# Kernel optimization log

Measured on AMD Instinct MI355X. Metric: run time of the kernel, lower is better.

The kernel has to match this reference:

```python
import jax, jax.numpy as jnp
import numpy as np

jax.config.update("jax_enable_x64", True)

B, N, M_EQ, D_INEQ = 64, 128, 32, 64
RHO = 1.0
THRES = 1e-5
MAX_ITERS = 5000  # safety cap (original loops until relative objective change <= 1e-5)


def setup_inputs() -> dict:
    key = jax.random.key(0)
    kL, kq, kG, kA, kx0, ks = jax.random.split(key, 6)
    L = jax.random.normal(kL, (B, N, N))
    Q = jnp.einsum('bij,bkj->bik', L, L) / N + jnp.eye(N)  # SPD, well-conditioned
    q = jax.random.normal(kq, (B, N))
    G = jax.random.normal(kG, (B, D_INEQ, N))
    A = jax.random.normal(kA, (B, M_EQ, N))
    x0 = jax.random.normal(kx0, (B, N))
    slack = jax.random.uniform(ks, (B, D_INEQ)) + 0.1
    h = jnp.einsum('bdn,bn->bd', G, x0) + slack  # strictly feasible ineq
    b = jnp.einsum('bmn,bn->bm', A, x0)          # feasible eq
    f32 = jnp.float32
    return {"Q": Q.astype(f32), "q": q.astype(f32), "G": G.astype(f32),
            "h": h.astype(f32), "A": A.astype(f32), "b": b.astype(f32)}


def _alt_diff_batch(Q, q, G, h, A, b):
    """Batched Alt-Diff ADMM QP solve; returns (x [B,n], dx/dq [B,n,n])."""
    Bb, n = q.shape
    d = h.shape[1]
    m = b.shape[1]
    dt = Q.dtype
    AtA = jnp.einsum('bmi,bmj->bij', A, A)
    GtG = jnp.einsum('bdi,bdj->bij', G, G)
    R = -jnp.linalg.inv(Q + RHO * AtA + RHO * GtG)
    ATb = RHO * jnp.einsum('bmn,bm->bn', A, b)
    GTh = RHO * jnp.einsum('bdn,bd->bn', G, h)
    eye = jnp.eye(n, dtype=dt)

    def obj(x):
        return 0.5 * jnp.einsum('bi,bij,bj->b', x, Q, x) + jnp.einsum('bi,bi->b', q, x)

    init = dict(
        xk=jnp.zeros((Bb, n), dt), sk=jnp.zeros((Bb, d), dt),
        lamb=jnp.zeros((Bb, m), dt), nu=jnp.zeros((Bb, d), dt),
        dxk=jnp.zeros((Bb, n, n), dt), dsk=jnp.zeros((Bb, d, n), dt),
        dlamb=jnp.zeros((Bb, m, n), dt), dnu=jnp.zeros((Bb, d, n), dt),
        res_prev=jnp.full((Bb,), 1000.0, dt),   # res = [1000, -100] init
        res_cur=jnp.full((Bb,), -100.0, dt),
        done=jnp.zeros((Bb,), bool),
        it=jnp.zeros((), jnp.int32),
    )

    def cond(s):
        return jnp.logical_and(jnp.any(~s["done"]), s["it"] < MAX_ITERS)

    def body(s):
        xk = jnp.einsum('bij,bj->bi', R,
                        q + jnp.einsum('bmn,bm->bn', A, s["lamb"])
                          + jnp.einsum('bdn,bd->bn', G, s["nu"]) - ATb
                          + RHO * jnp.einsum('bdn,bd->bn', G, s["sk"]) - GTh)
        dxk = jnp.einsum('bij,bjk->bik', R,
                         eye + jnp.einsum('bmn,bmk->bnk', A, s["dlamb"])
                             + jnp.einsum('bdn,bdk->bnk', G, s["dnu"])
                             + RHO * jnp.einsum('bdn,bdk->bnk', G, s["dsk"]))
        Gx = jnp.einsum('bdn,bn->bd', G, xk)
        sk = jax.nn.relu(-(1.0 / RHO) * s["nu"] - (Gx - h))
        sgn = (sk > 0).astype(dt)  # sgn applied to already-relu'd sk, as in source
        dsk = (-1.0 / RHO) * sgn[:, :, None] * (s["dnu"] + RHO * jnp.einsum('bdn,bnk->bdk', G, dxk))
        lamb = s["lamb"] + RHO * (jnp.einsum('bmn,bn->bm', A, xk) - b)
        dlamb = s["dlamb"] + RHO * jnp.einsum('bmn,bnk->bmk', A, dxk)
        nu = s["nu"] + RHO * (Gx + sk - h)
        dnu = s["dnu"] + RHO * (jnp.einsum('bdn,bnk->bdk', G, dxk) + dsk)
        res_new = obj(xk)

        keep = s["done"]

        def sel(old, new):
            mask = keep.reshape((-1,) + (1,) * (new.ndim - 1))
            return jnp.where(mask, old, new)

        res_prev = jnp.where(keep, s["res_prev"], s["res_cur"])
        res_cur = jnp.where(keep, s["res_cur"], res_new)
        done = keep | (jnp.abs((res_cur - res_prev) / res_prev) <= THRES)
        return dict(
            xk=sel(s["xk"], xk), sk=sel(s["sk"], sk),
            lamb=sel(s["lamb"], lamb), nu=sel(s["nu"], nu),
            dxk=sel(s["dxk"], dxk), dsk=sel(s["dsk"], dsk),
            dlamb=sel(s["dlamb"], dlamb), dnu=sel(s["dnu"], dnu),
            res_prev=res_prev, res_cur=res_cur, done=done, it=s["it"] + 1,
        )

    final = jax.lax.while_loop(cond, body, init)
    return final["xk"], final["dxk"]


def reference(Q, q, G, h, A, b):
    out_dtype = q.dtype
    f64 = jnp.float64
    x, _dx = _alt_diff_batch(Q.astype(f64), q.astype(f64), G.astype(f64),
                             h.astype(f64), A.astype(f64), b.astype(f64))
    return x.astype(out_dtype)
```

## Files before the change

### kernel.cpp

```cpp
#include <hip/hip_runtime.h>

#define NN 128
#define ME 32
#define DI 64
#define NZ 96
#define ROWD 130
#define MAXIT 5000

#define OFF_UN 16640
#define ROWB  (OFF_UN)
#define COLB  (OFF_UN + 256)
#define PPK   (OFF_UN)
#define TVX   (OFF_UN + 512)
#define TV16  (OFF_UN + 640)
#define FLG   (OFF_UN + 672)
#define YBUF  (OFF_UN)
#define KBUF  (OFF_UN + 1536)
#define CPART (OFF_UN + 1024)
#define VP    (OFF_UN + 1280)
#define BASEV (OFF_UN + 1792)
#define QBV   (OFF_UN + 1888)
#define FPART (OFF_UN + 1024)
#define RHSV  (OFF_UN + 1280)
#define XPART (OFF_UN + 1408)
#define CB    (OFF_UN + 2688)
#define QBUF  (OFF_UN + 2816)
#define V1    (OFF_UN + 2944)
#define V2    (OFF_UN + 3072)
#define HB    (OFF_UN + 3200)
#define BB    (OFF_UN + 3264)
#define CST   (OFF_UN + 3296)
#define ZBF   (OFF_UN + 3304)
#define LDS_DBL (OFF_UN + 3400)

typedef __attribute__((ext_vector_type(2))) float f32x2;

__device__ __forceinline__ float rlf(float v, int lane) {
  return __uint_as_float((unsigned)__builtin_amdgcn_readlane((int)__float_as_uint(v), lane));
}
__device__ __forceinline__ f32x2 fma2(f32x2 a, f32x2 b, f32x2 c) {
  return __builtin_elementwise_fma(a, b, c);
}

#define MV2(PA, ZS, L0) {                                                  \
    f32x2 z0 = { rlf(ZS, L0), rlf(ZS, (L0)+1) };                           \
    A0 = fma2(Kp[PA], z0, A0); B0 = fma2(Kp2[PA], z0, B0);                 \
    f32x2 z1 = { rlf(ZS, (L0)+2), rlf(ZS, (L0)+3) };                       \
    A1 = fma2(Kp[(PA)+1], z1, A1); B1 = fma2(Kp2[(PA)+1], z1, B1); }

#define CPYRANGE(LBASE, KBASE, CNT)                                        \
  _Pragma("unroll") for (int j = 0; j < (CNT); ++j) {                      \
    const int lj = (LBASE) + j, kc = (KBASE) + j;                          \
    float va = (float)ldsd[KBUF + kc*NZ + l];                              \
    float vb = (float)ldsd[KBUF + kc*NZ + 64 + lm];                        \
    if ((lj & 1) == 0) { Kp[lj>>1].x = va; Kp2[lj>>1].x = vb; }            \
    else               { Kp[lj>>1].y = va; Kp2[lj>>1].y = vb; }            \
  }

__global__ __launch_bounds__(256, 1) void altdiff_kernel(
    const float* __restrict__ Qg, const float* __restrict__ qg,
    const float* __restrict__ Gg, const float* __restrict__ hg,
    const float* __restrict__ Ag, const float* __restrict__ bg,
    float* __restrict__ out)
{
  extern __shared__ double ldsd[];

  const int bidx = blockIdx.x;
  const int tid  = threadIdx.x;
  const int w    = tid >> 6;
  const int l    = tid & 63;
  const int lm   = l & 31;
  const int ia   = tid & 127;
  const int hh   = tid >> 7;

  const float* Qb = Qg + (size_t)bidx * NN * NN;
  const float* Ab = Ag + (size_t)bidx * ME * NN;
  const float* Gb = Gg + (size_t)bidx * DI * NN;
  const float* qb = qg + (size_t)bidx * NN;
  const float* hb = hg + (size_t)bidx * DI;
  const float* bv = bg + (size_t)bidx * ME;

  if (tid < DI) ldsd[HB + tid] = (double)hb[tid];
  else if (tid < DI + ME) ldsd[BB + tid - DI] = (double)bv[tid - DI];
  if (tid >= 128) ldsd[QBUF + tid - 128] = (double)qb[tid - 128];

  const int r = tid >> 4, c = tid & 15;
  double acc[8][8];

  {
    const float4* Q4 = (const float4*)Qb;
#pragma unroll
    for (int rr = 0; rr < 8; ++rr) {
      float4 q0 = Q4[((8*r+rr) << 5) + 2*c];
      float4 q1 = Q4[((8*r+rr) << 5) + 2*c + 1];
      acc[rr][0]=(double)q0.x; acc[rr][1]=(double)q0.y; acc[rr][2]=(double)q0.z; acc[rr][3]=(double)q0.w;
      acc[rr][4]=(double)q1.x; acc[rr][5]=(double)q1.y; acc[rr][6]=(double)q1.z; acc[rr][7]=(double)q1.w;
    }
    const float4* A4 = (const float4*)Ab;
    for (int m = 0; m < ME; ++m) {
      float4 u0 = A4[(m << 5) + 2*r], u1 = A4[(m << 5) + 2*r + 1];
      float4 v0 = A4[(m << 5) + 2*c], v1 = A4[(m << 5) + 2*c + 1];
      double uu[8] = {(double)u0.x,(double)u0.y,(double)u0.z,(double)u0.w,
                      (double)u1.x,(double)u1.y,(double)u1.z,(double)u1.w};
      double vv[8] = {(double)v0.x,(double)v0.y,(double)v0.z,(double)v0.w,
                      (double)v1.x,(double)v1.y,(double)v1.z,(double)v1.w};
#pragma unroll
      for (int rr = 0; rr < 8; ++rr)
#pragma unroll
        for (int cc = 0; cc < 8; ++cc)
          acc[rr][cc] = fma(uu[rr], vv[cc], acc[rr][cc]);
    }
    const float4* G4 = (const float4*)Gb;
    for (int d = 0; d < DI; ++d) {
      float4 u0 = G4[(d << 5) + 2*r], u1 = G4[(d << 5) + 2*r + 1];
      float4 v0 = G4[(d << 5) + 2*c], v1 = G4[(d << 5) + 2*c + 1];
      double uu[8] = {(double)u0.x,(double)u0.y,(double)u0.z,(double)u0.w,
                      (double)u1.x,(double)u1.y,(double)u1.z,(double)u1.w};
      double vv[8] = {(double)v0.x,(double)v0.y,(double)v0.z,(double)v0.w,
                      (double)v1.x,(double)v1.y,(double)v1.z,(double)v1.w};
#pragma unroll
      for (int rr = 0; rr < 8; ++rr)
#pragma unroll
        for (int cc = 0; cc < 8; ++cc)
          acc[rr][cc] = fma(uu[rr], vv[cc], acc[rr][cc]);
    }
  }

  {
    if (r == 0) {
#pragma unroll
      for (int cc = 0; cc < 8; ++cc) ldsd[ROWB + 8*c + cc] = acc[0][cc];
    }
    if (c == 0) {
#pragma unroll
      for (int rr = 0; rr < 8; ++rr) ldsd[COLB + 8*r + rr] = acc[rr][0];
    }
    __syncthreads();
    for (int k = 0; k < NN; ++k) {
      const int pb = (k & 1) << 7;
      const int krt = k >> 3, kcl = k & 7;
      double rowk[8], colv[8];
#pragma unroll
      for (int cc = 0; cc < 8; ++cc) rowk[cc] = ldsd[ROWB + pb + 8*c + cc];
#pragma unroll
      for (int rr = 0; rr < 8; ++rr) colv[rr] = ldsd[COLB + pb + 8*r + rr];
      const double dkk  = ldsd[ROWB + pb + k];
      const double rcpd = 1.0 / dkk;
      double rdv[8];
#pragma unroll
      for (int cc = 0; cc < 8; ++cc) rdv[cc] = rowk[cc] * rcpd;
      const bool pivR = (r == krt), pivC = (c == krt);
#pragma unroll
      for (int rr = 0; rr < 8; ++rr) {
        const double cv = colv[rr] * rcpd;
        const bool pr = pivR && (rr == kcl);
#pragma unroll
        for (int cc = 0; cc < 8; ++cc) {
          double gen = fma(-cv, rowk[cc], acc[rr][cc]);
          acc[rr][cc] = pr ? rdv[cc] : gen;
        }
      }
      if (pivC) {
#pragma unroll
        for (int cc = 0; cc < 8; ++cc) if (cc == kcl) {
#pragma unroll
          for (int rr = 0; rr < 8; ++rr) {
            const bool pr2 = pivR && (rr == kcl);
            acc[rr][cc] = pr2 ? -rcpd : colv[rr] * rcpd;
          }
        }
      }
      if (k < NN - 1) {
        const int pb2 = ((k + 1) & 1) << 7;
        const int krt2 = (k + 1) >> 3, kcl2 = (k + 1) & 7;
        if (r == krt2) {
#pragma unroll
          for (int rr = 0; rr < 8; ++rr) if (rr == kcl2) {
#pragma unroll
            for (int cc = 0; cc < 8; ++cc) ldsd[ROWB + pb2 + 8*c + cc] = acc[rr][cc];
          }
        }
        if (c == krt2) {
#pragma unroll
          for (int cc = 0; cc < 8; ++cc) if (cc == kcl2) {
#pragma unroll
            for (int rr = 0; rr < 8; ++rr) ldsd[COLB + pb2 + 8*r + rr] = acc[rr][cc];
          }
        }
      }
      __syncthreads();
    }
#pragma unroll
    for (int rr = 0; rr < 8; ++rr) {
      double2* dst = (double2*)(ldsd + (8*r+rr)*ROWD + 8*c);
#pragma unroll
      for (int t = 0; t < 4; ++t) dst[t] = make_double2(acc[rr][2*t], acc[rr][2*t+1]);
    }
  }
  __syncthreads();

  f32x2 Kp[14], Kp2[14];
  for (int blk = 0; blk < 8; ++blk) {
    {
      const float* gp[6];
#pragma unroll
      for (int jj = 0; jj < 6; ++jj) {
        int it = 12*blk + 6*hh + jj;
        gp[jj] = (it < DI) ? (Gb + it*NN) : (Ab + (it - DI)*NN);
      }
      double a2[6] = {0,0,0,0,0,0};
#pragma unroll 4
      for (int t = 0; t < NN; ++t) {
        double rv = ldsd[t*ROWD + ia];
#pragma unroll
        for (int jj = 0; jj < 6; ++jj)
          a2[jj] = fma(rv, (double)gp[jj][t], a2[jj]);
      }
      double2* yst = (double2*)(ldsd + YBUF + ia*12 + 6*hh);
#pragma unroll
      for (int p = 0; p < 3; ++p) yst[p] = make_double2(a2[2*p], a2[2*p+1]);
    }
    __syncthreads();
    {
      const int r2 = (ia < NZ) ? ia : 0;
      const float* brow = (r2 < DI) ? (Gb + r2*NN) : (Ab + (r2 - DI)*NN);
      double a2[6] = {0,0,0,0,0,0};
#pragma unroll 4
      for (int t = 0; t < NN; ++t) {
        double bvv = (double)brow[t];
        const double2* yr = (const double2*)(ldsd + YBUF + t*12 + 6*hh);
        double2 y0 = yr[0], y1 = yr[1], y2 = yr[2];
        a2[0] = fma(bvv, y0.x, a2[0]); a2[1] = fma(bvv, y0.y, a2[1]);
        a2[2] = fma(bvv, y1.x, a2[2]); a2[3] = fma(bvv, y1.y, a2[3]);
        a2[4] = fma(bvv, y2.x, a2[4]); a2[5] = fma(bvv, y2.y, a2[5]);
      }
      if (ia < NZ) {
#pragma unroll
        for (int jj = 0; jj < 6; ++jj) ldsd[KBUF + (6*hh + jj)*NZ + ia] = a2[jj];
      }
    }
    __syncthreads();
    if (w == 0) {
      if (blk == 0)      { CPYRANGE(0,  0, 12) }
      else if (blk == 1) { CPYRANGE(12, 0, 12) }
      else if (blk == 2) { CPYRANGE(24, 0, 4) }
    } else if (w == 1) {
      if (blk == 2)      { CPYRANGE(0,  4, 8) }
      else if (blk == 3) { CPYRANGE(8,  0, 12) }
      else if (blk == 4) { CPYRANGE(20, 0, 8) }
    } else if (w == 2) {
      if (blk == 4)      { CPYRANGE(0,  8, 4) }
      else if (blk == 5) { CPYRANGE(4,  0, 12) }
      else if (blk == 6) { CPYRANGE(16, 0, 8) }
    } else {
      if (blk == 6)      { CPYRANGE(0,  8, 4) }
      else if (blk == 7) { CPYRANGE(4,  0, 12) }
    }
    __syncthreads();
  }

  {
    double s = 0;
#pragma unroll 8
    for (int jc = 0; jc < 48; ++jc) {
      int j = 48*hh + jc;
      double coef = (j < DI) ? ldsd[HB + j] : ldsd[BB + j - DI];
      const float* src = (j < DI) ? (Gb + j*NN) : (Ab + (j - DI)*NN);
      s = fma(-(double)src[ia], coef, s);
    }
    ldsd[CPART + hh*128 + ia] = s;
  }
  __syncthreads();
  if (tid < NN) ldsd[CB + tid] = ldsd[QBUF + tid] + ldsd[CPART + tid] + ldsd[CPART + 128 + tid];
  __syncthreads();

  {
    double a = 0, b2 = 0;
#pragma unroll 4
    for (int tt = 0; tt < 64; ++tt) {
      int t = 64*hh + tt;
      double rv = ldsd[t*ROWD + ia];
      a  = fma(rv, ldsd[CB + t], a);
      b2 = fma(rv, ldsd[QBUF + t], b2);
    }
    ldsd[VP + hh*128 + ia] = a;
    ldsd[VP + 256 + hh*128 + ia] = b2;
  }
  __syncthreads();
  if (tid < NN) {
    ldsd[V1 + tid] = ldsd[VP + tid] + ldsd[VP + 128 + tid];
    ldsd[V2 + tid] = ldsd[VP + 256 + tid] + ldsd[VP + 384 + tid];
  }
  __syncthreads();

  {
    const int r2 = (ia < NZ) ? ia : 0;
    const float* brow = (r2 < DI) ? (Gb + r2*NN) : (Ab + (r2 - DI)*NN);
    const int voff = hh ? V2 : V1;
    double s = 0;
#pragma unroll 4
    for (int t = 0; t < NN; ++t) s = fma((double)brow[t], ldsd[voff + t], s);
    if (ia < NZ) ldsd[(hh ? QBV : BASEV) + ia] = s;
  }
  if (w == 0) {
    double pc = ldsd[V1+l]*ldsd[CB+l]   + ldsd[V1+64+l]*ldsd[CB+64+l];
    double pq = ldsd[V1+l]*ldsd[QBUF+l] + ldsd[V1+64+l]*ldsd[QBUF+64+l];
#pragma unroll
    for (int off = 32; off >= 1; off >>= 1) { pc += __shfl_xor(pc, off); pq += __shfl_xor(pq, off); }
    if (l == 0) { ldsd[CST] = pc; ldsd[CST+1] = pq; }
  }
  __syncthreads();

  const double baseA = ldsd[BASEV + l];
  const double baseB = ldsd[BASEV + 64 + lm];
  const double qvA   = ldsd[QBV + l];
  const double qvB   = ldsd[QBV + 64 + lm];
  const double hb2   = ldsd[HB + l] - baseA;
  const double bb2   = baseB - ldsd[BB + lm];
  const double S_uc  = ldsd[CST], S_qu = ldsd[CST + 1];
  double hnb = hb2, lb = bb2;
  float hnbf = (float)hnb, lbf = (float)lb;
  float zplo = 0.f, zphi = 0.f;
  float zAlo = 0.f, zAhi = 0.f, zBlo = 0.f, zBhi = 0.f, zClo = 0.f, zChi = 0.f;
  double res_prev = 1000.0, res_cur = -100.0;

  {
    *(float2*)&ldsd[PPK + w*64 + l] = make_float2(0.f, 0.f);
    if (tid == 0) { ldsd[FLG] = 0.0; ldsd[FLG + 1] = 0.0; }
  }

  for (int it = 0; it < MAXIT + 3; ++it) {
    __syncthreads();
    const int buf = it & 1, nbuf = buf ^ 1;
    const int bprev = nbuf;
    const double fl = ldsd[FLG + bprev];
    const float2* pb = (const float2*)(ldsd + PPK + buf*256);
    float2 p0 = pb[l], p1 = pb[64 + l], p2 = pb[128 + l], p3 = pb[192 + l];
    double a0 = 0, a1 = 0, a2 = 0, a3 = 0;
    double t1v[16];
    if (w == 3) {
      const int g = l & 15;
      const double* tq = ldsd + TVX + bprev*64;
      a0 = tq[g]; a1 = tq[g + 16]; a2 = tq[g + 32]; a3 = tq[g + 48];
      const double2* tp = (const double2*)(ldsd + TV16 + bprev*16);
#pragma unroll
      for (int u = 0; u < 8; ++u) { double2 vv = tp[u]; t1v[2*u] = vv.x; t1v[2*u+1] = vv.y; }
    }
    float slo = (p0.x + p1.x) + (p2.x + p3.x);
    float tf   = hnbf - slo;
    float zflo = fabsf(tf);
    float shi = 0.f, zfhi = 0.f;
    if (w >= 2) {
      shi  = (p0.y + p1.y) + (p2.y + p3.y);
      zfhi = lbf + shi;
    }
    if (it >= 3 && fl != 0.0) break;
    if (w == 3) { zClo = zBlo; zChi = zBhi; zBlo = zAlo; zBhi = zAhi; zAlo = zplo; zAhi = zphi; }
    if (it < MAXIT) {
      double t = hnb - (double)slo;
      hnb = hb2 + fmin(t, 0.0);
      hnbf = (float)hnb;
      if (w >= 2) {
        double lamn = lb + (double)shi;
        lb = lamn + bb2;
        lbf = (float)lb;
      }
      if (w == 3) { zplo = zflo; zphi = zfhi; }
      f32x2 A0 = {0.f, 0.f}, A1 = A0, B0 = A0, B1 = A0;
      if (w == 0) {
        MV2(0,  zflo, 0)  MV2(2,  zflo, 4)  MV2(4,  zflo, 8)  MV2(6,  zflo, 12)
        MV2(8,  zflo, 16) MV2(10, zflo, 20) MV2(12, zflo, 24)
      } else if (w == 1) {
        MV2(0,  zflo, 28) MV2(2,  zflo, 32) MV2(4,  zflo, 36) MV2(6,  zflo, 40)
        MV2(8,  zflo, 44) MV2(10, zflo, 48) MV2(12, zflo, 52)
      } else if (w == 2) {
        MV2(0,  zflo, 56) MV2(2,  zflo, 60)
        MV2(4,  zfhi, 0)  MV2(6,  zfhi, 4)  MV2(8,  zfhi, 8)  MV2(10, zfhi, 12)
      } else {
        MV2(0,  zfhi, 16) MV2(2,  zfhi, 20) MV2(4,  zfhi, 24) MV2(6,  zfhi, 28)
      }
      f32x2 As = A0 + A1, Bs = B0 + B1;
      *(float2*)&ldsd[PPK + nbuf*256 + w*64 + l] = make_float2(As.x + As.y, Bs.x + Bs.y);
      if (w == 3) {
        double yf  = (double)slo + baseA;
        double zAl = (double)zAlo;
        double tvl = fma(qvA, zAl, -0.5*(zAl*(baseA + yf) + yf*yf));
        double yfB = (double)shi + baseB;
        double zAh = (double)zAhi;
        double tvh = fma(qvB, zAh, -0.5*(zAh*(baseB + yfB) + yfB*yfB));
        ldsd[TVX + buf*64 + l] = tvl + ((l < 32) ? tvh : 0.0);
      }
    }
    if (w == 3) {
      if (l < 16 && it >= 1 && it <= MAXIT)
        ldsd[TV16 + buf*16 + l] = (a0 + a1) + (a2 + a3);
      if (it >= 2 && it <= MAXIT + 1) {
        double s1 = ((t1v[0] + t1v[1]) + (t1v[2] + t1v[3])) + ((t1v[4] + t1v[5]) + (t1v[6] + t1v[7]));
        double s2 = ((t1v[8] + t1v[9]) + (t1v[10] + t1v[11])) + ((t1v[12] + t1v[13]) + (t1v[14] + t1v[15]));
        double obj = (s1 + s2) - 0.5*S_uc + S_qu;
        res_prev = res_cur; res_cur = obj;
        if (l == 0)
          ldsd[FLG + buf] = (fabs(res_cur - res_prev) <= 1e-5 * fabs(res_prev)) ? 1.0 : 0.0;
      }
    }
  }

  if (w == 3) {
    ldsd[ZBF + l] = (double)zClo;
    if (l < 32) ldsd[ZBF + 64 + l] = (double)zChi;
  }
  __syncthreads();
  {
    double s = 0;
#pragma unroll 8
    for (int jc = 0; jc < 48; ++jc) {
      int j = 48*hh + jc;
      double zj = ldsd[ZBF + j];
      const float* src = (j < DI) ? (Gb + j*NN) : (Ab + (j - DI)*NN);
      s = fma((double)src[ia], zj, s);
    }
    ldsd[FPART + hh*128 + ia] = s;
  }
  __syncthreads();
  if (tid < NN) ldsd[RHSV + tid] = ldsd[CB + tid] + ldsd[FPART + tid] + ldsd[FPART + 128 + tid];
  __syncthreads();
  {
    double s = 0;
#pragma unroll 4
    for (int tt = 0; tt < 64; ++tt) {
      int t = 64*hh + tt;
      s = fma(ldsd[t*ROWD + ia], ldsd[RHSV + t], s);
    }
    ldsd[XPART + hh*128 + ia] = s;
  }
  __syncthreads();
  if (tid < NN)
    out[(size_t)bidx * NN + tid] = (float)(ldsd[XPART + tid] + ldsd[XPART + 128 + tid]);
}

extern "C" void kernel_launch(void* const* d_in, const int* in_sizes, int n_in,
                              void* d_out, int out_size, void* d_ws, size_t ws_size,
                              hipStream_t stream) {
  (void)in_sizes; (void)n_in; (void)out_size; (void)d_ws; (void)ws_size;
  const float* Q = (const float*)d_in[0];
  const float* q = (const float*)d_in[1];
  const float* G = (const float*)d_in[2];
  const float* h = (const float*)d_in[3];
  const float* A = (const float*)d_in[4];
  const float* b = (const float*)d_in[5];
  float* out = (float*)d_out;
  const size_t lds_bytes = (size_t)LDS_DBL * sizeof(double);
  altdiff_kernel<<<dim3(64), dim3(256), lds_bytes, stream>>>(Q, q, G, h, A, b, out);
}
```

Measured before the change: 685.9 us.

## Process two QP problems per workgroup with interleaved ADMM iterations

Each workgroup now handles two batch elements. It builds both problems' operators into separate register sets, then runs their ADMM iterations interleaved in one loop, so the serial per-iteration latency chain of one problem can hide the other's. The final solve uses a precomputed R*B^T stored in the workspace instead of recomputing it. This halves the grid to 32 blocks, doubles the register pressure and the setup work done per block, and adds global workspace traffic.

Result: slower. 1.297 ms (+89.0%).

```diff
diff --git a/kernel.cpp b/kernel.cpp
--- a/kernel.cpp
+++ b/kernel.cpp
@@ -7,31 +7,34 @@
 #define ROWD 130
 #define MAXIT 5000
 
+#define PPK_A   0
+#define PPK_B   384
+#define ZEXLF_A 1536
+#define ZEXHF_A 1664
+#define ZEXLF_B 1728
+#define ZEXHF_B 1856
+#define TVX_A   960
+#define TVX_B   1088
+#define TV16_A  1216
+#define TV16_B  1248
+#define FLG_A   1280
+#define FLG_B   1282
+#define ZBF_A   1284
+#define ZBF_B   1380
 #define OFF_UN 16640
 #define ROWB  (OFF_UN)
 #define COLB  (OFF_UN + 256)
-#define PPK   (OFF_UN)
-#define TVX   (OFF_UN + 512)
-#define TV16  (OFF_UN + 640)
-#define FLG   (OFF_UN + 672)
 #define YBUF  (OFF_UN)
-#define KBUF  (OFF_UN + 1536)
-#define CPART (OFF_UN + 1024)
-#define VP    (OFF_UN + 1280)
-#define BASEV (OFF_UN + 1792)
-#define QBV   (OFF_UN + 1888)
-#define FPART (OFF_UN + 1024)
-#define RHSV  (OFF_UN + 1280)
-#define XPART (OFF_UN + 1408)
-#define CB    (OFF_UN + 2688)
-#define QBUF  (OFF_UN + 2816)
-#define V1    (OFF_UN + 2944)
-#define V2    (OFF_UN + 3072)
-#define HB    (OFF_UN + 3200)
-#define BB    (OFF_UN + 3264)
-#define CST   (OFF_UN + 3296)
-#define ZBF   (OFF_UN + 3304)
-#define LDS_DBL (OFF_UN + 3400)
+#define KBUFF (2*(OFF_UN + 1536))
+#define CPART (OFF_UN)
+#define CBT   (OFF_UN + 256)
+#define QBUF  (OFF_UN + 384)
+#define VP    (OFF_UN + 512)
+#define V2T   (OFF_UN + 1024)
+#define FPART (OFF_UN)
+#define PBASE (OFF_UN + 2112)
+#define PCH   418
+#define LDS_DBL (PBASE + 2*PCH)
 
 typedef __attribute__((ext_vector_type(2))) float f32x2;
 
@@ -42,28 +45,55 @@
   return __builtin_elementwise_fma(a, b, c);
 }
 
-#define MV2(PA, ZS, L0) {                                                  \
-    f32x2 z0 = { rlf(ZS, L0), rlf(ZS, (L0)+1) };                           \
-    A0 = fma2(Kp[PA], z0, A0); B0 = fma2(Kp2[PA], z0, B0);                 \
-    f32x2 z1 = { rlf(ZS, (L0)+2), rlf(ZS, (L0)+3) };                       \
-    A1 = fma2(Kp[(PA)+1], z1, A1); B1 = fma2(Kp2[(PA)+1], z1, B1); }
-
-#define CPYRANGE(LBASE, KBASE, CNT)                                        \
-  _Pragma("unroll") for (int j = 0; j < (CNT); ++j) {                      \
-    const int lj = (LBASE) + j, kc = (KBASE) + j;                          \
-    float va = (float)ldsd[KBUF + kc*NZ + l];                              \
-    float vb = (float)ldsd[KBUF + kc*NZ + 64 + lm];                        \
-    if ((lj & 1) == 0) { Kp[lj>>1].x = va; Kp2[lj>>1].x = vb; }            \
-    else               { Kp[lj>>1].y = va; Kp2[lj>>1].y = vb; }            \
+#define MV2(KP, KP2, PA, ZS, L0) {                                          \
+    f32x2 z0 = { rlf(ZS, L0), rlf(ZS, (L0)+1) };                            \
+    A0 = fma2(KP[PA], z0, A0); B0 = fma2(KP2[PA], z0, B0);                  \
+    f32x2 z1 = { rlf(ZS, (L0)+2), rlf(ZS, (L0)+3) };                        \
+    A1 = fma2(KP[(PA)+1], z1, A1); B1 = fma2(KP2[(PA)+1], z1, B1); }
+
+#define BURST_LO_A(KP, KP2, Z)                              \
+    MV2(KP,KP2,0,Z,0)  MV2(KP,KP2,2,Z,4)  MV2(KP,KP2,4,Z,8)  MV2(KP,KP2,6,Z,12) \
+    MV2(KP,KP2,8,Z,16) MV2(KP,KP2,10,Z,20) MV2(KP,KP2,12,Z,24) MV2(KP,KP2,14,Z,28)
+#define BURST_LO_B(KP, KP2, Z)                             \
+    MV2(KP,KP2,0,Z,32) MV2(KP,KP2,2,Z,36) MV2(KP,KP2,4,Z,40) MV2(KP,KP2,6,Z,44) \
+    MV2(KP,KP2,8,Z,48) MV2(KP,KP2,10,Z,52) MV2(KP,KP2,12,Z,56) MV2(KP,KP2,14,Z,60)
+#define BURST_HI(KP, KP2, Z)                             \
+    MV2(KP,KP2,0,Z,0)  MV2(KP,KP2,2,Z,4)  MV2(KP,KP2,4,Z,8)  MV2(KP,KP2,6,Z,12) \
+    MV2(KP,KP2,8,Z,16) MV2(KP,KP2,10,Z,20) MV2(KP,KP2,12,Z,24) MV2(KP,KP2,14,Z,28)
+
+#define CPYRANGE(KP, KP2, LBASE, KBASE, CNT)                                \
+  _Pragma("unroll") for (int j = 0; j < (CNT); ++j) {                       \
+    const int lj = (LBASE) + j, kc = (KBASE) + j;                           \
+    float va = ldsf[KBUFF + kc*NZ + l];                                     \
+    float vb = ldsf[KBUFF + kc*NZ + 64 + lm];                               \
+    if ((lj & 1) == 0) { KP[lj>>1].x = va; KP2[lj>>1].x = vb; }             \
+    else               { KP[lj>>1].y = va; KP2[lj>>1].y = vb; }             \
+  }
+
+#define KCOPY_ARMS(KP, KP2)                                                 \
+  if (w == 0) {                                                             \
+    if (blk == 0)      { CPYRANGE(KP,KP2,0,  0, 12) }                       \
+    else if (blk == 1) { CPYRANGE(KP,KP2,12, 0, 12) }                       \
+    else if (blk == 2) { CPYRANGE(KP,KP2,24, 0, 8) }                        \
+  } else if (w == 1) {                                                      \
+    if (blk == 2)      { CPYRANGE(KP,KP2,0,  8, 4) }                        \
+    else if (blk == 3) { CPYRANGE(KP,KP2,4,  0, 12) }                       \
+    else if (blk == 4) { CPYRANGE(KP,KP2,16, 0, 12) }                       \
+    else if (blk == 5) { CPYRANGE(KP,KP2,28, 0, 4) }                        \
+  } else if (w == 2) {                                                      \
+    if (blk == 5)      { CPYRANGE(KP,KP2,0,  4, 8) }                        \
+    else if (blk == 6) { CPYRANGE(KP,KP2,8,  0, 12) }                       \
+    else if (blk == 7) { CPYRANGE(KP,KP2,20, 0, 12) }                       \
   }
 
 __global__ __launch_bounds__(256, 1) void altdiff_kernel(
     const float* __restrict__ Qg, const float* __restrict__ qg,
     const float* __restrict__ Gg, const float* __restrict__ hg,
     const float* __restrict__ Ag, const float* __restrict__ bg,
-    float* __restrict__ out)
+    float* __restrict__ out, float* __restrict__ wsf)
 {
   extern __shared__ double ldsd[];
+  float* const ldsf = (float*)ldsd;
 
   const int bidx = blockIdx.x;
   const int tid  = threadIdx.x;
@@ -72,376 +102,468 @@
   const int lm   = l & 31;
   const int ia   = tid & 127;
   const int hh   = tid >> 7;
-
-  const float* Qb = Qg + (size_t)bidx * NN * NN;
-  const float* Ab = Ag + (size_t)bidx * ME * NN;
-  const float* Gb = Gg + (size_t)bidx * DI * NN;
-  const float* qb = qg + (size_t)bidx * NN;
-  const float* hb = hg + (size_t)bidx * DI;
-  const float* bv = bg + (size_t)bidx * ME;
-
-  if (tid < DI) ldsd[HB + tid] = (double)hb[tid];
-  else if (tid < DI + ME) ldsd[BB + tid - DI] = (double)bv[tid - DI];
-  if (tid >= 128) ldsd[QBUF + tid - 128] = (double)qb[tid - 128];
-
   const int r = tid >> 4, c = tid & 15;
-  double acc[8][8];
-
-  {
-    const float4* Q4 = (const float4*)Qb;
-#pragma unroll
-    for (int rr = 0; rr < 8; ++rr) {
-      float4 q0 = Q4[((8*r+rr) << 5) + 2*c];
-      float4 q1 = Q4[((8*r+rr) << 5) + 2*c + 1];
-      acc[rr][0]=(double)q0.x; acc[rr][1]=(double)q0.y; acc[rr][2]=(double)q0.z; acc[rr][3]=(double)q0.w;
-      acc[rr][4]=(double)q1.x; acc[rr][5]=(double)q1.y; acc[rr][6]=(double)q1.z; acc[rr][7]=(double)q1.w;
-    }
-    const float4* A4 = (const float4*)Ab;
-    for (int m = 0; m < ME; ++m) {
-      float4 u0 = A4[(m << 5) + 2*r], u1 = A4[(m << 5) + 2*r + 1];
-      float4 v0 = A4[(m << 5) + 2*c], v1 = A4[(m << 5) + 2*c + 1];
-      double uu[8] = {(double)u0.x,(double)u0.y,(double)u0.z,(double)u0.w,
-                      (double)u1.x,(double)u1.y,(double)u1.z,(double)u1.w};
-      double vv[8] = {(double)v0.x,(double)v0.y,(double)v0.z,(double)v0.w,
-                      (double)v1.x,(double)v1.y,(double)v1.z,(double)v1.w};
-#pragma unroll
-      for (int rr = 0; rr < 8; ++rr)
-#pragma unroll
-        for (int cc = 0; cc < 8; ++cc)
-          acc[rr][cc] = fma(uu[rr], vv[cc], acc[rr][cc]);
-    }
-    const float4* G4 = (const float4*)Gb;
-    for (int d = 0; d < DI; ++d) {
-      float4 u0 = G4[(d << 5) + 2*r], u1 = G4[(d << 5) + 2*r + 1];
-      float4 v0 = G4[(d << 5) + 2*c], v1 = G4[(d << 5) + 2*c + 1];
-      double uu[8] = {(double)u0.x,(double)u0.y,(double)u0.z,(double)u0.w,
-                      (double)u1.x,(double)u1.y,(double)u1.z,(double)u1.w};
-      double vv[8] = {(double)v0.x,(double)v0.y,(double)v0.z,(double)v0.w,
-                      (double)v1.x,(double)v1.y,(double)v1.z,(double)v1.w};
-#pragma unroll
-      for (int rr = 0; rr < 8; ++rr)
-#pragma unroll
-        for (int cc = 0; cc < 8; ++cc)
-          acc[rr][cc] = fma(uu[rr], vv[cc], acc[rr][cc]);
-    }
-  }
-
-  {
-    if (r == 0) {
-#pragma unroll
-      for (int cc = 0; cc < 8; ++cc) ldsd[ROWB + 8*c + cc] = acc[0][cc];
-    }
-    if (c == 0) {
-#pragma unroll
-      for (int rr = 0; rr < 8; ++rr) ldsd[COLB + 8*r + rr] = acc[rr][0];
-    }
-    __syncthreads();
-    for (int k = 0; k < NN; ++k) {
-      const int pb = (k & 1) << 7;
-      const int krt = k >> 3, kcl = k & 7;
-      double rowk[8], colv[8];
-#pragma unroll
-      for (int cc = 0; cc < 8; ++cc) rowk[cc] = ldsd[ROWB + pb + 8*c + cc];
-#pragma unroll
-      for (int rr = 0; rr < 8; ++rr) colv[rr] = ldsd[COLB + pb + 8*r + rr];
-      const double dkk  = ldsd[ROWB + pb + k];
-      const double rcpd = 1.0 / dkk;
-      double rdv[8];
-#pragma unroll
-      for (int cc = 0; cc < 8; ++cc) rdv[cc] = rowk[cc] * rcpd;
-      const bool pivR = (r == krt), pivC = (c == krt);
+
+  f32x2 KpA[16], Kp2A[16], KpB[16], Kp2B[16];
+
+  for (int g = 0; g < 2; ++g) {
+    const int ch = 2*bidx + g;
+    const float* Qb = Qg + (size_t)ch * NN * NN;
+    const float* Ab = Ag + (size_t)ch * ME * NN;
+    const float* Gb = Gg + (size_t)ch * DI * NN;
+    const float* qb = qg + (size_t)ch * NN;
+    const float* hb = hg + (size_t)ch * DI;
+    const float* bv = bg + (size_t)ch * ME;
+    const int PG = PBASE + g*PCH;
+
+    if (tid < DI) ldsd[PG + tid] = (double)hb[tid];
+    else if (tid < DI + ME) ldsd[PG + 64 + tid - DI] = (double)bv[tid - DI];
+
+    double acc[8][8];
+    {
+      const float4* Q4 = (const float4*)Qb;
 #pragma unroll
       for (int rr = 0; rr < 8; ++rr) {
-        const double cv = colv[rr] * rcpd;
-        const bool pr = pivR && (rr == kcl);
-#pragma unroll
-        for (int cc = 0; cc < 8; ++cc) {
-          double gen = fma(-cv, rowk[cc], acc[rr][cc]);
-          acc[rr][cc] = pr ? rdv[cc] : gen;
-        }
-      }
-      if (pivC) {
-#pragma unroll
-        for (int cc = 0; cc < 8; ++cc) if (cc == kcl) {
-#pragma unroll
-          for (int rr = 0; rr < 8; ++rr) {
-            const bool pr2 = pivR && (rr == kcl);
-            acc[rr][cc] = pr2 ? -rcpd : colv[rr] * rcpd;
+        float4 q0 = Q4[((8*r+rr) << 5) + 2*c];
+        float4 q1 = Q4[((8*r+rr) << 5) + 2*c + 1];
+        acc[rr][0]=(double)q0.x; acc[rr][1]=(double)q0.y; acc[rr][2]=(double)q0.z; acc[rr][3]=(double)q0.w;
+        acc[rr][4]=(double)q1.x; acc[rr][5]=(double)q1.y; acc[rr][6]=(double)q1.z; acc[rr][7]=(double)q1.w;
+      }
+      const float4* A4 = (const float4*)Ab;
+      for (int m = 0; m < ME; ++m) {
+        float4 u0 = A4[(m << 5) + 2*r], u1 = A4[(m << 5) + 2*r + 1];
+        float4 v0 = A4[(m << 5) + 2*c], v1 = A4[(m << 5) + 2*c + 1];
+        double uu[8] = {(double)u0.x,(double)u0.y,(double)u0.z,(double)u0.w,
+                        (double)u1.x,(double)u1.y,(double)u1.z,(double)u1.w};
+        double vv[8] = {(double)v0.x,(double)v0.y,(double)v0.z,(double)v0.w,
+                        (double)v1.x,(double)v1.y,(double)v1.z,(double)v1.w};
+#pragma unroll
+        for (int rr = 0; rr < 8; ++rr)
+#pragma unroll
+          for (int cc = 0; cc < 8; ++cc)
+            acc[rr][cc] = fma(uu[rr], vv[cc], acc[rr][cc]);
+      }
+      const float4* G4 = (const float4*)Gb;
+      for (int d = 0; d < DI; ++d) {
+        float4 u0 = G4[(d << 5) + 2*r], u1 = G4[(d << 5) + 2*r + 1];
+        float4 v0 = G4[(d << 5) + 2*c], v1 = G4[(d << 5) + 2*c + 1];
+        double uu[8] = {(double)u0.x,(double)u0.y,(double)u0.z,(double)u0.w,
+                        (double)u1.x,(double)u1.y,(double)u1.z,(double)u1.w};
+        double vv[8] = {(double)v0.x,(double)v0.y,(double)v0.z,(double)v0.w,
+                        (double)v1.x,(double)v1.y,(double)v1.z,(double)v1.w};
+#pragma unroll
+        for (int rr = 0; rr < 8; ++rr)
+#pragma unroll
+          for (int cc = 0; cc < 8; ++cc)
+            acc[rr][cc] = fma(uu[rr], vv[cc], acc[rr][cc]);
+      }
+    }
+
+    {
+      if (r == 0) {
+#pragma unroll
+        for (int cc = 0; cc < 8; ++cc) ldsd[ROWB + 8*c + cc] = acc[0][cc];
+      }
+      if (c == 0) {
+#pragma unroll
+        for (int rr = 0; rr < 8; ++rr) ldsd[COLB + 8*r + rr] = acc[rr][0];
+      }
+      __syncthreads();
+      for (int k = 0; k < NN; ++k) {
+        const int pb = (k & 1) << 7;
+        const int krt = k >> 3, kcl = k & 7;
+        double rowk[8], colv[8];
+#pragma unroll
+        for (int cc = 0; cc < 8; ++cc) rowk[cc] = ldsd[ROWB + pb + 8*c + cc];
+#pragma unroll
+        for (int rr = 0; rr < 8; ++rr) colv[rr] = ldsd[COLB + pb + 8*r + rr];
+        const double dkk  = ldsd[ROWB + pb + k];
+        const double rcpd = 1.0 / dkk;
+        double rdv[8];
+#pragma unroll
+        for (int cc = 0; cc < 8; ++cc) rdv[cc] = rowk[cc] * rcpd;
+        const bool pivR = (r == krt), pivC = (c == krt);
+#pragma unroll
+        for (int rr = 0; rr < 8; ++rr) {
+          const double cv = colv[rr] * rcpd;
+          const bool pr = pivR && (rr == kcl);
+#pragma unroll
+          for (int cc = 0; cc < 8; ++cc) {
+            double gen = fma(-cv, rowk[cc], acc[rr][cc]);
+            acc[rr][cc] = pr ? rdv[cc] : gen;
           }
         }
-      }
-      if (k < NN - 1) {
-        const int pb2 = ((k + 1) & 1) << 7;
-        const int krt2 = (k + 1) >> 3, kcl2 = (k + 1) & 7;
-        if (r == krt2) {
-#pragma unroll
-          for (int rr = 0; rr < 8; ++rr) if (rr == kcl2) {
-#pragma unroll
-            for (int cc = 0; cc < 8; ++cc) ldsd[ROWB + pb2 + 8*c + cc] = acc[rr][cc];
+        if (pivC) {
+#pragma unroll
+          for (int cc = 0; cc < 8; ++cc) if (cc == kcl) {
+#pragma unroll
+            for (int rr = 0; rr < 8; ++rr) {
+              const bool pr2 = pivR && (rr == kcl);
+              acc[rr][cc] = pr2 ? -rcpd : colv[rr] * rcpd;
+            }
           }
         }
-        if (c == krt2) {
-#pragma unroll
-          for (int cc = 0; cc < 8; ++cc) if (cc == kcl2) {
-#pragma unroll
-            for (int rr = 0; rr < 8; ++rr) ldsd[COLB + pb2 + 8*r + rr] = acc[rr][cc];
+        if (k < NN - 1) {
+          const int pb2 = ((k + 1) & 1) << 7;
+          const int krt2 = (k + 1) >> 3, kcl2 = (k + 1) & 7;
+          if (r == krt2) {
+#pragma unroll
+            for (int rr = 0; rr < 8; ++rr) if (rr == kcl2) {
+#pragma unroll
+              for (int cc = 0; cc < 8; ++cc) ldsd[ROWB + pb2 + 8*c + cc] = acc[rr][cc];
+            }
           }
-        }
+          if (c == krt2) {
+#pragma unroll
+            for (int cc = 0; cc < 8; ++cc) if (cc == kcl2) {
+#pragma unroll
+              for (int rr = 0; rr < 8; ++rr) ldsd[COLB + pb2 + 8*r + rr] = acc[rr][cc];
+            }
+          }
+        }
+        __syncthreads();
+      }
+#pragma unroll
+      for (int rr = 0; rr < 8; ++rr) {
+        double2* dst = (double2*)(ldsd + (8*r+rr)*ROWD + 8*c);
+#pragma unroll
+        for (int t = 0; t < 4; ++t) dst[t] = make_double2(acc[rr][2*t], acc[rr][2*t+1]);
+      }
+    }
+    __syncthreads();
+
+    for (int blk = 0; blk < 8; ++blk) {
+      {
+        const float* gp[6];
+#pragma unroll
+        for (int jj = 0; jj < 6; ++jj) {
+          int it = 12*blk + 6*hh + jj;
+          gp[jj] = (it < DI) ? (Gb + it*NN) : (Ab + (it - DI)*NN);
+        }
+        double a2[6] = {0,0,0,0,0,0};
+#pragma unroll 4
+        for (int t = 0; t < NN; ++t) {
+          double rv = ldsd[t*ROWD + ia];
+#pragma unroll
+          for (int jj = 0; jj < 6; ++jj)
+            a2[jj] = fma(rv, (double)gp[jj][t], a2[jj]);
+        }
+        double2* yst = (double2*)(ldsd + YBUF + ia*12 + 6*hh);
+#pragma unroll
+        for (int p = 0; p < 3; ++p) yst[p] = make_double2(a2[2*p], a2[2*p+1]);
+        float* rbt = wsf + (size_t)ch * (96*128);
+#pragma unroll
+        for (int jj = 0; jj < 6; ++jj)
+          rbt[(12*blk + 6*hh + jj)*128 + ia] = (float)a2[jj];
       }
       __syncthreads();
-    }
-#pragma unroll
-    for (int rr = 0; rr < 8; ++rr) {
-      double2* dst = (double2*)(ldsd + (8*r+rr)*ROWD + 8*c);
-#pragma unroll
-      for (int t = 0; t < 4; ++t) dst[t] = make_double2(acc[rr][2*t], acc[rr][2*t+1]);
-    }
-  }
-  __syncthreads();
-
-  f32x2 Kp[14], Kp2[14];
-  for (int blk = 0; blk < 8; ++blk) {
+      {
+        const int r2 = (ia < NZ) ? ia : 0;
+        const float* brow = (r2 < DI) ? (Gb + r2*NN) : (Ab + (r2 - DI)*NN);
+        double a2[6] = {0,0,0,0,0,0};
+#pragma unroll 4
+        for (int t = 0; t < NN; ++t) {
+          double bvv = (double)brow[t];
+          const double2* yr = (const double2*)(ldsd + YBUF + t*12 + 6*hh);
+          double2 y0 = yr[0], y1 = yr[1], y2 = yr[2];
+          a2[0] = fma(bvv, y0.x, a2[0]); a2[1] = fma(bvv, y0.y, a2[1]);
+          a2[2] = fma(bvv, y1.x, a2[2]); a2[3] = fma(bvv, y1.y, a2[3]);
+          a2[4] = fma(bvv, y2.x, a2[4]); a2[5] = fma(bvv, y2.y, a2[5]);
+        }
+        if (ia < NZ) {
+#pragma unroll
+          for (int jj = 0; jj < 6; ++jj) ldsf[KBUFF + (6*hh + jj)*NZ + ia] = (float)a2[jj];
+        }
+      }
+      __syncthreads();
+      if (g == 0) { KCOPY_ARMS(KpA, Kp2A) } else { KCOPY_ARMS(KpB, Kp2B) }
+      __syncthreads();
+    }
+
+    if (tid < NN) ldsd[QBUF + tid] = (double)qb[tid];
     {
-      const float* gp[6];
-#pragma unroll
-      for (int jj = 0; jj < 6; ++jj) {
-        int it = 12*blk + 6*hh + jj;
-        gp[jj] = (it < DI) ? (Gb + it*NN) : (Ab + (it - DI)*NN);
-      }
-      double a2[6] = {0,0,0,0,0,0};
+      double s = 0;
+#pragma unroll 8
+      for (int jc = 0; jc < 48; ++jc) {
+        int j = 48*hh + jc;
+        double coef = (j < DI) ? ldsd[PG + j] : ldsd[PG + 64 + j - DI];
+        const float* src = (j < DI) ? (Gb + j*NN) : (Ab + (j - DI)*NN);
+        s = fma(-(double)src[ia], coef, s);
+      }
+      ldsd[CPART + hh*128 + ia] = s;
+    }
+    __syncthreads();
+    if (tid < NN) ldsd[CBT + tid] = ldsd[QBUF + tid] + ldsd[CPART + tid] + ldsd[CPART + 128 + tid];
+    __syncthreads();
+
+    {
+      double a = 0, b2 = 0;
 #pragma unroll 4
-      for (int t = 0; t < NN; ++t) {
+      for (int tt = 0; tt < 64; ++tt) {
+        int t = 64*hh + tt;
         double rv = ldsd[t*ROWD + ia];
-#pragma unroll
-        for (int jj = 0; jj < 6; ++jj)
-          a2[jj] = fma(rv, (double)gp[jj][t], a2[jj]);
-      }
-      double2* yst = (double2*)(ldsd + YBUF + ia*12 + 6*hh);
-#pragma unroll
-      for (int p = 0; p < 3; ++p) yst[p] = make_double2(a2[2*p], a2[2*p+1]);
-    }
-    __syncthreads();
+        a  = fma(rv, ldsd[CBT + t], a);
+        b2 = fma(rv, ldsd[QBUF + t], b2);
+      }
+      ldsd[VP + hh*128 + ia] = a;
+      ldsd[VP + 256 + hh*128 + ia] = b2;
+    }
+    __syncthreads();
+    if (tid < NN) {
+      ldsd[PG + 288 + tid] = ldsd[VP + tid] + ldsd[VP + 128 + tid];
+      ldsd[V2T + tid]      = ldsd[VP + 256 + tid] + ldsd[VP + 384 + tid];
+    }
+    __syncthreads();
+
     {
       const int r2 = (ia < NZ) ? ia : 0;
       const float* brow = (r2 < DI) ? (Gb + r2*NN) : (Ab + (r2 - DI)*NN);
-      double a2[6] = {0,0,0,0,0,0};
+      const int voff = hh ? V2T : (PG + 288);
+      double s = 0;
 #pragma unroll 4
-      for (int t = 0; t < NN; ++t) {
-        double bvv = (double)brow[t];
-        const double2* yr = (const double2*)(ldsd + YBUF + t*12 + 6*hh);
-        double2 y0 = yr[0], y1 = yr[1], y2 = yr[2];
-        a2[0] = fma(bvv, y0.x, a2[0]); a2[1] = fma(bvv, y0.y, a2[1]);
-        a2[2] = fma(bvv, y1.x, a2[2]); a2[3] = fma(bvv, y1.y, a2[3]);
-        a2[4] = fma(bvv, y2.x, a2[4]); a2[5] = fma(bvv, y2.y, a2[5]);
-      }
-      if (ia < NZ) {
-#pragma unroll
-        for (int jj = 0; jj < 6; ++jj) ldsd[KBUF + (6*hh + jj)*NZ + ia] = a2[jj];
-      }
-    }
-    __syncthreads();
+      for (int t = 0; t < NN; ++t) s = fma((double)brow[t], ldsd[voff + t], s);
+      if (ia < NZ) ldsd[(hh ? (PG + 192) : (PG + 96)) + ia] = s;
+    }
     if (w == 0) {
-      if (blk == 0)      { CPYRANGE(0,  0, 12) }
-      else if (blk == 1) { CPYRANGE(12, 0, 12) }
-      else if (blk == 2) { CPYRANGE(24, 0, 4) }
+      double pc = ldsd[PG+288+l]*ldsd[CBT+l]  + ldsd[PG+288+64+l]*ldsd[CBT+64+l];
+      double pq = ldsd[PG+288+l]*ldsd[QBUF+l] + ldsd[PG+288+64+l]*ldsd[QBUF+64+l];
+#pragma unroll
+      for (int off = 32; off >= 1; off >>= 1) { pc += __shfl_xor(pc, off); pq += __shfl_xor(pq, off); }
+      if (l == 0) { ldsd[PG + 416] = pc; ldsd[PG + 417] = pq; }
+    }
+    __syncthreads();
+  }
+
+  const int PA_ = PBASE, PB_ = PBASE + PCH;
+  const double baseA_lo = ldsd[PA_+96 + l],  baseA_hi = ldsd[PA_+96 + 64 + lm];
+  const double qvA_lo   = ldsd[PA_+192 + l], qvA_hi   = ldsd[PA_+192 + 64 + lm];
+  const double hbA2 = ldsd[PA_ + l] - baseA_lo;
+  const double bbA2 = baseA_hi - ldsd[PA_+64 + lm];
+  const double S_ucA = ldsd[PA_+416], S_quA = ldsd[PA_+417];
+  const double baseB_lo = ldsd[PB_+96 + l],  baseB_hi = ldsd[PB_+96 + 64 + lm];
+  const double qvB_lo   = ldsd[PB_+192 + l], qvB_hi   = ldsd[PB_+192 + 64 + lm];
+  const double hbB2 = ldsd[PB_ + l] - baseB_lo;
+  const double bbB2 = baseB_hi - ldsd[PB_+64 + lm];
+  const double S_ucB = ldsd[PB_+416], S_quB = ldsd[PB_+417];
+
+  double hnbA = hbA2, lbA = bbA2, hnbB = hbB2, lbB = bbB2;
+  float hnbfA = (float)hnbA, lbfA = (float)lbA, hnbfB = (float)hnbB, lbfB = (float)lbB;
+  float2 ownA = make_float2(0.f, 0.f), ownB = make_float2(0.f, 0.f);
+  float zAfA_lo=0.f, zAfA_hi=0.f, zBfA_lo=0.f, zBfA_hi=0.f, zCfA_lo=0.f, zCfA_hi=0.f;
+  float zAfB_lo=0.f, zAfB_hi=0.f, zBfB_lo=0.f, zBfB_hi=0.f, zCfB_lo=0.f, zCfB_hi=0.f;
+  double res_prevA = 1000.0, res_curA = -100.0, res_prevB = 1000.0, res_curB = -100.0;
+  bool doneA = false, doneB = false;
+
+  {
+    if (w < 3) {
+      *(float2*)&ldsd[PPK_A + w*64 + l] = make_float2(0.f, 0.f);
+      *(float2*)&ldsd[PPK_B + w*64 + l] = make_float2(0.f, 0.f);
+    }
+    if (w == 0) { ldsf[ZEXLF_A + 64 + l] = 0.f; ldsf[ZEXLF_B + 64 + l] = 0.f; }
+    if (w == 2 && l < 32) { ldsf[ZEXHF_A + 32 + l] = 0.f; ldsf[ZEXHF_B + 32 + l] = 0.f; }
+    if (tid == 0) { ldsd[FLG_A] = 0.0; ldsd[FLG_A+1] = 0.0; ldsd[FLG_B] = 0.0; ldsd[FLG_B+1] = 0.0; }
+  }
+
+  for (int it = 0; it < MAXIT + 3; ++it) {
+    __syncthreads();
+    const int buf = it & 1, nbuf = buf ^ 1;
+    const int bprev = nbuf;
+    const double flA = ldsd[FLG_A + bprev];
+    const double flB = ldsd[FLG_B + bprev];
+    const float2* pbA = (const float2*)(ldsd + PPK_A + buf*192);
+    const float2* pbB = (const float2*)(ldsd + PPK_B + buf*192);
+
+    if (w == 0) {
+      float2 a1v = pbA[64 + l], a2v = pbA[128 + l];
+      float2 b1v = pbB[64 + l], b2v = pbB[128 + l];
+      float sloA = (ownA.x + a1v.x) + a2v.x;
+      float zfA  = fabsf(hnbfA - sloA);
+      float sloB = (ownB.x + b1v.x) + b2v.x;
+      float zfB  = fabsf(hnbfB - sloB);
+      doneA = doneA || (it >= 3 && flA != 0.0);
+      doneB = doneB || (it >= 3 && flB != 0.0);
+      if (doneA && doneB) break;
+      if (!doneA && it < MAXIT) {
+        ldsf[ZEXLF_A + buf*64 + l] = zfA;
+        double t = hnbA - (double)sloA; hnbA = hbA2 + fmin(t, 0.0); hnbfA = (float)hnbA;
+        f32x2 A0 = {0.f,0.f}, A1 = A0, B0 = A0, B1 = A0;
+        BURST_LO_A(KpA, Kp2A, zfA)
+        f32x2 As = A0 + A1, Bs = B0 + B1;
+        float2 np = make_float2(As.x + As.y, Bs.x + Bs.y);
+        *(float2*)&ldsd[PPK_A + nbuf*192 + l] = np;  ownA = np;
+      }
+      if (!doneB && it < MAXIT) {
+        ldsf[ZEXLF_B + buf*64 + l] = zfB;
+        double t = hnbB - (double)sloB; hnbB = hbB2 + fmin(t, 0.0); hnbfB = (float)hnbB;
+        f32x2 A0 = {0.f,0.f}, A1 = A0, B0 = A0, B1 = A0;
+        BURST_LO_A(KpB, Kp2B, zfB)
+        f32x2 As = A0 + A1, Bs = B0 + B1;
+        float2 np = make_float2(As.x + As.y, Bs.x + Bs.y);
+        *(float2*)&ldsd[PPK_B + nbuf*192 + l] = np;  ownB = np;
+      }
     } else if (w == 1) {
-      if (blk == 2)      { CPYRANGE(0,  4, 8) }
-      else if (blk == 3) { CPYRANGE(8,  0, 12) }
-      else if (blk == 4) { CPYRANGE(20, 0, 8) }
+      float2 a0v = pbA[l], a2v = pbA[128 + l];
+      float2 b0v = pbB[l], b2v = pbB[128 + l];
+      float sloA = (a0v.x + ownA.x) + a2v.x;
+      float zfA  = fabsf(hnbfA - sloA);
+      float sloB = (b0v.x + ownB.x) + b2v.x;
+      float zfB  = fabsf(hnbfB - sloB);
+      doneA = doneA || (it >= 3 && flA != 0.0);
+      doneB = doneB || (it >= 3 && flB != 0.0);
+      if (doneA && doneB) break;
+      if (!doneA && it < MAXIT) {
+        double t = hnbA - (double)sloA; hnbA = hbA2 + fmin(t, 0.0); hnbfA = (float)hnbA;
+        f32x2 A0 = {0.f,0.f}, A1 = A0, B0 = A0, B1 = A0;
+        BURST_LO_B(KpA, Kp2A, zfA)
+        f32x2 As = A0 + A1, Bs = B0 + B1;
+        float2 np = make_float2(As.x + As.y, Bs.x + Bs.y);
+        *(float2*)&ldsd[PPK_A + nbuf*192 + 64 + l] = np;  ownA = np;
+      }
+      if (!doneB && it < MAXIT) {
+        double t = hnbB - (double)sloB; hnbB = hbB2 + fmin(t, 0.0); hnbfB = (float)hnbB;
+        f32x2 A0 = {0.f,0.f}, A1 = A0, B0 = A0, B1 = A0;
+        BURST_LO_B(KpB, Kp2B, zfB)
+        f32x2 As = A0 + A1, Bs = B0 + B1;
+        float2 np = make_float2(As.x + As.y, Bs.x + Bs.y);
+        *(float2*)&ldsd[PPK_B + nbuf*192 + 64 + l] = np;  ownB = np;
+      }
     } else if (w == 2) {
-      if (blk == 4)      { CPYRANGE(0,  8, 4) }
-      else if (blk == 5) { CPYRANGE(4,  0, 12) }
-      else if (blk == 6) { CPYRANGE(16, 0, 8) }
+      float2 a0v = pbA[l], a1v = pbA[64 + l];
+      float2 b0v = pbB[l], b1v = pbB[64 + l];
+      float shiA = (a0v.y + a1v.y) + ownA.y;
+      float zfA  = lbfA + shiA;
+      float shiB = (b0v.y + b1v.y) + ownB.y;
+      float zfB  = lbfB + shiB;
+      doneA = doneA || (it >= 3 && flA != 0.0);
+      doneB = doneB || (it >= 3 && flB != 0.0);
+      if (doneA && doneB) break;
+      if (!doneA && it < MAXIT) {
+        if (l < 32) ldsf[ZEXHF_A + buf*32 + l] = zfA;
+        double lamn = lbA + (double)shiA; lbA = lamn + bbA2; lbfA = (float)lbA;
+        f32x2 A0 = {0.f,0.f}, A1 = A0, B0 = A0, B1 = A0;
+        BURST_HI(KpA, Kp2A, zfA)
+        f32x2 As = A0 + A1, Bs = B0 + B1;
+        float2 np = make_float2(As.x + As.y, Bs.x + Bs.y);
+        *(float2*)&ldsd[PPK_A + nbuf*192 + 128 + l] = np;  ownA = np;
+      }
+      if (!doneB && it < MAXIT) {
+        if (l < 32) ldsf[ZEXHF_B + buf*32 + l] = zfB;
+        double lamn = lbB + (double)shiB; lbB = lamn + bbB2; lbfB = (float)lbB;
+        f32x2 A0 = {0.f,0.f}, A1 = A0, B0 = A0, B1 = A0;
+        BURST_HI(KpB, Kp2B, zfB)
+        f32x2 As = A0 + A1, Bs = B0 + B1;
+        float2 np = make_float2(As.x + As.y, Bs.x + Bs.y);
+        *(float2*)&ldsd[PPK_B + nbuf*192 + 128 + l] = np;  ownB = np;
+      }
     } else {
-      if (blk == 6)      { CPYRANGE(0,  8, 4) }
-      else if (blk == 7) { CPYRANGE(4,  0, 12) }
-    }
-    __syncthreads();
-  }
-
-  {
+      float2 vA0 = pbA[l], vA1 = pbA[64 + l], vA2 = pbA[128 + l];
+      float2 vB0 = pbB[l], vB1 = pbB[64 + l], vB2 = pbB[128 + l];
+      const float ztlA = ldsf[ZEXLF_A + bprev*64 + l];
+      const float zthA = ldsf[ZEXHF_A + bprev*32 + lm];
+      const float ztlB = ldsf[ZEXLF_B + bprev*64 + l];
+      const float zthB = ldsf[ZEXHF_B + bprev*32 + lm];
+      const int g2 = l & 15;
+      const double* tqA = ldsd + TVX_A + bprev*64;
+      double aA0 = tqA[g2], aA1 = tqA[g2+16], aA2 = tqA[g2+32], aA3 = tqA[g2+48];
+      const double* tqB = ldsd + TVX_B + bprev*64;
+      double aB0 = tqB[g2], aB1 = tqB[g2+16], aB2 = tqB[g2+32], aB3 = tqB[g2+48];
+      double t1A[16], t1B[16];
+      {
+        const double2* tpA = (const double2*)(ldsd + TV16_A + bprev*16);
+        const double2* tpB = (const double2*)(ldsd + TV16_B + bprev*16);
+#pragma unroll
+        for (int u = 0; u < 8; ++u) {
+          double2 va = tpA[u]; t1A[2*u] = va.x; t1A[2*u+1] = va.y;
+          double2 vb = tpB[u]; t1B[2*u] = vb.x; t1B[2*u+1] = vb.y;
+        }
+      }
+      doneA = doneA || (it >= 3 && flA != 0.0);
+      doneB = doneB || (it >= 3 && flB != 0.0);
+      if (doneA && doneB) break;
+      if (!doneA) {
+        zCfA_lo = zBfA_lo; zCfA_hi = zBfA_hi; zBfA_lo = zAfA_lo; zBfA_hi = zAfA_hi;
+        zAfA_lo = ztlA;    zAfA_hi = zthA;
+        if (it < MAXIT) {
+          float slo_f = (vA0.x + vA1.x) + vA2.x;
+          float shi_f = (vA0.y + vA1.y) + vA2.y;
+          double zAl = (double)zAfA_lo;
+          double yf  = (double)slo_f + baseA_lo;
+          double tvl = fma(qvA_lo, zAl, -0.5*(zAl*(baseA_lo + yf) + yf*yf));
+          double zAh = (double)zAfA_hi;
+          double yfB = (double)shi_f + baseA_hi;
+          double tvh = fma(qvA_hi, zAh, -0.5*(zAh*(baseA_hi + yfB) + yfB*yfB));
+          ldsd[TVX_A + buf*64 + l] = tvl + ((l < 32) ? tvh : 0.0);
+        }
+        if (l < 16 && it >= 1 && it <= MAXIT)
+          ldsd[TV16_A + buf*16 + l] = (aA0 + aA1) + (aA2 + aA3);
+        if (it >= 2 && it <= MAXIT + 1) {
+          double s1 = ((t1A[0]+t1A[1]) + (t1A[2]+t1A[3])) + ((t1A[4]+t1A[5]) + (t1A[6]+t1A[7]));
+          double s2 = ((t1A[8]+t1A[9]) + (t1A[10]+t1A[11])) + ((t1A[12]+t1A[13]) + (t1A[14]+t1A[15]));
+          double obj = (s1 + s2) - 0.5*S_ucA + S_quA;
+          res_prevA = res_curA; res_curA = obj;
+          if (l == 0)
+            ldsd[FLG_A + buf] = (fabs(res_curA - res_prevA) <= 1e-5 * fabs(res_prevA)) ? 1.0 : 0.0;
+        }
+      }
+      if (!doneB) {
+        zCfB_lo = zBfB_lo; zCfB_hi = zBfB_hi; zBfB_lo = zAfB_lo; zBfB_hi = zAfB_hi;
+        zAfB_lo = ztlB;    zAfB_hi = zthB;
+        if (it < MAXIT) {
+          float slo_f = (vB0.x + vB1.x) + vB2.x;
+          float shi_f = (vB0.y + vB1.y) + vB2.y;
+          double zAl = (double)zAfB_lo;
+          double yf  = (double)slo_f + baseB_lo;
+          double tvl = fma(qvB_lo, zAl, -0.5*(zAl*(baseB_lo + yf) + yf*yf));
+          double zAh = (double)zAfB_hi;
+          double yfB = (double)shi_f + baseB_hi;
+          double tvh = fma(qvB_hi, zAh, -0.5*(zAh*(baseB_hi + yfB) + yfB*yfB));
+          ldsd[TVX_B + buf*64 + l] = tvl + ((l < 32) ? tvh : 0.0);
+        }
+        if (l < 16 && it >= 1 && it <= MAXIT)
+          ldsd[TV16_B + buf*16 + l] = (aB0 + aB1) + (aB2 + aB3);
+        if (it >= 2 && it <= MAXIT + 1) {
+          double s1 = ((t1B[0]+t1B[1]) + (t1B[2]+t1B[3])) + ((t1B[4]+t1B[5]) + (t1B[6]+t1B[7]));
+          double s2 = ((t1B[8]+t1B[9]) + (t1B[10]+t1B[11])) + ((t1B[12]+t1B[13]) + (t1B[14]+t1B[15]));
+          double obj = (s1 + s2) - 0.5*S_ucB + S_quB;
+          res_prevB = res_curB; res_curB = obj;
+          if (l == 0)
+            ldsd[FLG_B + buf] = (fabs(res_curB - res_prevB) <= 1e-5 * fabs(res_prevB)) ? 1.0 : 0.0;
+        }
+      }
+    }
+  }
+
+  if (w == 3) {
+    ldsd[ZBF_A + l] = (double)zCfA_lo;
+    if (l < 32) ldsd[ZBF_A + 64 + l] = (double)zCfA_hi;
+    ldsd[ZBF_B + l] = (double)zCfB_lo;
+    if (l < 32) ldsd[ZBF_B + 64 + l] = (double)zCfB_hi;
+  }
+  __syncthreads();
+  for (int g = 0; g < 2; ++g) {
+    const float* rbt = wsf + (size_t)(2*bidx + g) * (96*128);
+    const int ZB = g ? ZBF_B : ZBF_A;
     double s = 0;
 #pragma unroll 8
     for (int jc = 0; jc < 48; ++jc) {
       int j = 48*hh + jc;
-      double coef = (j < DI) ? ldsd[HB + j] : ldsd[BB + j - DI];
-      const float* src = (j < DI) ? (Gb + j*NN) : (Ab + (j - DI)*NN);
-      s = fma(-(double)src[ia], coef, s);
-    }
-    ldsd[CPART + hh*128 + ia] = s;
-  }
-  __syncthreads();
-  if (tid < NN) ldsd[CB + tid] = ldsd[QBUF + tid] + ldsd[CPART + tid] + ldsd[CPART + 128 + tid];
-  __syncthreads();
-
-  {
-    double a = 0, b2 = 0;
-#pragma unroll 4
-    for (int tt = 0; tt < 64; ++tt) {
-      int t = 64*hh + tt;
-      double rv = ldsd[t*ROWD + ia];
-      a  = fma(rv, ldsd[CB + t], a);
-      b2 = fma(rv, ldsd[QBUF + t], b2);
-    }
-    ldsd[VP + hh*128 + ia] = a;
-    ldsd[VP + 256 + hh*128 + ia] = b2;
-  }
-  __syncthreads();
-  if (tid < NN) {
-    ldsd[V1 + tid] = ldsd[VP + tid] + ldsd[VP + 128 + tid];
-    ldsd[V2 + tid] = ldsd[VP + 256 + tid] + ldsd[VP + 384 + tid];
-  }
-  __syncthreads();
-
-  {
-    const int r2 = (ia < NZ) ? ia : 0;
-    const float* brow = (r2 < DI) ? (Gb + r2*NN) : (Ab + (r2 - DI)*NN);
-    const int voff = hh ? V2 : V1;
-    double s = 0;
-#pragma unroll 4
-    for (int t = 0; t < NN; ++t) s = fma((double)brow[t], ldsd[voff + t], s);
-    if (ia < NZ) ldsd[(hh ? QBV : BASEV) + ia] = s;
-  }
-  if (w == 0) {
-    double pc = ldsd[V1+l]*ldsd[CB+l]   + ldsd[V1+64+l]*ldsd[CB+64+l];
-    double pq = ldsd[V1+l]*ldsd[QBUF+l] + ldsd[V1+64+l]*ldsd[QBUF+64+l];
-#pragma unroll
-    for (int off = 32; off >= 1; off >>= 1) { pc += __shfl_xor(pc, off); pq += __shfl_xor(pq, off); }
-    if (l == 0) { ldsd[CST] = pc; ldsd[CST+1] = pq; }
-  }
-  __syncthreads();
-
-  const double baseA = ldsd[BASEV + l];
-  const double baseB = ldsd[BASEV + 64 + lm];
-  const double qvA   = ldsd[QBV + l];
-  const double qvB   = ldsd[QBV + 64 + lm];
-  const double hb2   = ldsd[HB + l] - baseA;
-  const double bb2   = baseB - ldsd[BB + lm];
-  const double S_uc  = ldsd[CST], S_qu = ldsd[CST + 1];
-  double hnb = hb2, lb = bb2;
-  float hnbf = (float)hnb, lbf = (float)lb;
-  float zplo = 0.f, zphi = 0.f;
-  float zAlo = 0.f, zAhi = 0.f, zBlo = 0.f, zBhi = 0.f, zClo = 0.f, zChi = 0.f;
-  double res_prev = 1000.0, res_cur = -100.0;
-
-  {
-    *(float2*)&ldsd[PPK + w*64 + l] = make_float2(0.f, 0.f);
-    if (tid == 0) { ldsd[FLG] = 0.0; ldsd[FLG + 1] = 0.0; }
-  }
-
-  for (int it = 0; it < MAXIT + 3; ++it) {
-    __syncthreads();
-    const int buf = it & 1, nbuf = buf ^ 1;
-    const int bprev = nbuf;
-    const double fl = ldsd[FLG + bprev];
-    const float2* pb = (const float2*)(ldsd + PPK + buf*256);
-    float2 p0 = pb[l], p1 = pb[64 + l], p2 = pb[128 + l], p3 = pb[192 + l];
-    double a0 = 0, a1 = 0, a2 = 0, a3 = 0;
-    double t1v[16];
-    if (w == 3) {
-      const int g = l & 15;
-      const double* tq = ldsd + TVX + bprev*64;
-      a0 = tq[g]; a1 = tq[g + 16]; a2 = tq[g + 32]; a3 = tq[g + 48];
-      const double2* tp = (const double2*)(ldsd + TV16 + bprev*16);
-#pragma unroll
-      for (int u = 0; u < 8; ++u) { double2 vv = tp[u]; t1v[2*u] = vv.x; t1v[2*u+1] = vv.y; }
-    }
-    float slo = (p0.x + p1.x) + (p2.x + p3.x);
-    float tf   = hnbf - slo;
-    float zflo = fabsf(tf);
-    float shi = 0.f, zfhi = 0.f;
-    if (w >= 2) {
-      shi  = (p0.y + p1.y) + (p2.y + p3.y);
-      zfhi = lbf + shi;
-    }
-    if (it >= 3 && fl != 0.0) break;
-    if (w == 3) { zClo = zBlo; zChi = zBhi; zBlo = zAlo; zBhi = zAhi; zAlo = zplo; zAhi = zphi; }
-    if (it < MAXIT) {
-      double t = hnb - (double)slo;
-      hnb = hb2 + fmin(t, 0.0);
-      hnbf = (float)hnb;
-      if (w >= 2) {
-        double lamn = lb + (double)shi;
-        lb = lamn + bb2;
-        lbf = (float)lb;
-      }
-      if (w == 3) { zplo = zflo; zphi = zfhi; }
-      f32x2 A0 = {0.f, 0.f}, A1 = A0, B0 = A0, B1 = A0;
-      if (w == 0) {
-        MV2(0,  zflo, 0)  MV2(2,  zflo, 4)  MV2(4,  zflo, 8)  MV2(6,  zflo, 12)
-        MV2(8,  zflo, 16) MV2(10, zflo, 20) MV2(12, zflo, 24)
-      } else if (w == 1) {
-        MV2(0,  zflo, 28) MV2(2,  zflo, 32) MV2(4,  zflo, 36) MV2(6,  zflo, 40)
-        MV2(8,  zflo, 44) MV2(10, zflo, 48) MV2(12, zflo, 52)
-      } else if (w == 2) {
-        MV2(0,  zflo, 56) MV2(2,  zflo, 60)
-        MV2(4,  zfhi, 0)  MV2(6,  zfhi, 4)  MV2(8,  zfhi, 8)  MV2(10, zfhi, 12)
-      } else {
-        MV2(0,  zfhi, 16) MV2(2,  zfhi, 20) MV2(4,  zfhi, 24) MV2(6,  zfhi, 28)
-      }
-      f32x2 As = A0 + A1, Bs = B0 + B1;
-      *(float2*)&ldsd[PPK + nbuf*256 + w*64 + l] = make_float2(As.x + As.y, Bs.x + Bs.y);
-      if (w == 3) {
-        double yf  = (double)slo + baseA;
-        double zAl = (double)zAlo;
-        double tvl = fma(qvA, zAl, -0.5*(zAl*(baseA + yf) + yf*yf));
-        double yfB = (double)shi + baseB;
-        double zAh = (double)zAhi;
-        double tvh = fma(qvB, zAh, -0.5*(zAh*(baseB + yfB) + yfB*yfB));
-        ldsd[TVX + buf*64 + l] = tvl + ((l < 32) ? tvh : 0.0);
-      }
-    }
-    if (w == 3) {
-      if (l < 16 && it >= 1 && it <= MAXIT)
-        ldsd[TV16 + buf*16 + l] = (a0 + a1) + (a2 + a3);
-      if (it >= 2 && it <= MAXIT + 1) {
-        double s1 = ((t1v[0] + t1v[1]) + (t1v[2] + t1v[3])) + ((t1v[4] + t1v[5]) + (t1v[6] + t1v[7]));
-        double s2 = ((t1v[8] + t1v[9]) + (t1v[10] + t1v[11])) + ((t1v[12] + t1v[13]) + (t1v[14] + t1v[15]));
-        double obj = (s1 + s2) - 0.5*S_uc + S_qu;
-        res_prev = res_cur; res_cur = obj;
-        if (l == 0)
-          ldsd[FLG + buf] = (fabs(res_cur - res_prev) <= 1e-5 * fabs(res_prev)) ? 1.0 : 0.0;
-      }
-    }
-  }
-
-  if (w == 3) {
-    ldsd[ZBF + l] = (double)zClo;
-    if (l < 32) ldsd[ZBF + 64 + l] = (double)zChi;
-  }
-  __syncthreads();
-  {
-    double s = 0;
-#pragma unroll 8
-    for (int jc = 0; jc < 48; ++jc) {
-      int j = 48*hh + jc;
-      double zj = ldsd[ZBF + j];
-      const float* src = (j < DI) ? (Gb + j*NN) : (Ab + (j - DI)*NN);
-      s = fma((double)src[ia], zj, s);
+      s = fma((double)rbt[j*128 + ia], ldsd[ZB + j], s);
     }
     ldsd[FPART + hh*128 + ia] = s;
-  }
-  __syncthreads();
-  if (tid < NN) ldsd[RHSV + tid] = ldsd[CB + tid] + ldsd[FPART + tid] + ldsd[FPART + 128 + tid];
-  __syncthreads();
-  {
-    double s = 0;
-#pragma unroll 4
-    for (int tt = 0; tt < 64; ++tt) {
-      int t = 64*hh + tt;
-      s = fma(ldsd[t*ROWD + ia], ldsd[RHSV + t], s);
-    }
-    ldsd[XPART + hh*128 + ia] = s;
-  }
-  __syncthreads();
-  if (tid < NN)
-    out[(size_t)bidx * NN + tid] = (float)(ldsd[XPART + tid] + ldsd[XPART + 128 + tid]);
+    __syncthreads();
+    if (tid < NN) {
+      const int V1g = PBASE + g*PCH + 288;
+      out[(size_t)(2*bidx + g)*NN + tid] =
+          (float)(ldsd[V1g + tid] + ldsd[FPART + tid] + ldsd[FPART + 128 + tid]);
+    }
+    __syncthreads();
+  }
 }
 
 extern "C" void kernel_launch(void* const* d_in, const int* in_sizes, int n_in,
                               void* d_out, int out_size, void* d_ws, size_t ws_size,
                               hipStream_t stream) {
-  (void)in_sizes; (void)n_in; (void)out_size; (void)d_ws; (void)ws_size;
+  (void)in_sizes; (void)n_in; (void)out_size; (void)ws_size;
   const float* Q = (const float*)d_in[0];
   const float* q = (const float*)d_in[1];
   const float* G = (const float*)d_in[2];
@@ -449,6 +571,7 @@
   const float* A = (const float*)d_in[4];
   const float* b = (const float*)d_in[5];
   float* out = (float*)d_out;
+  float* ws  = (float*)d_ws;
   const size_t lds_bytes = (size_t)LDS_DBL * sizeof(double);
-  altdiff_kernel<<<dim3(64), dim3(256), lds_bytes, stream>>>(Q, q, G, h, A, b, out);
+  altdiff_kernel<<<dim3(32), dim3(256), lds_bytes, stream>>>(Q, q, G, h, A, b, out, ws);
 }
```
